# Kernel tuning notes

Hardware: AMD Instinct MI355X
Metric: run time of the kernel (lower is better)

The kernel has to match this reference:

```python
import jax, jax.numpy as jnp
import numpy as np

D = 256
H = 16
HD = D // H
N_BIAS = 6
B, E = 8, 1024


def _layernorm(x, g, b, eps=1e-5):
    mu = jnp.mean(x, axis=-1, keepdims=True)
    var = jnp.mean(jnp.square(x - mu), axis=-1, keepdims=True)
    return (x - mu) * jax.lax.rsqrt(var + eps) * g + b


def setup_inputs() -> dict:
    key = jax.random.key(0)
    ks = jax.random.split(key, 16)
    s = 0.02
    inp = {
        "x": jax.random.normal(ks[0], (B, E, D), dtype=jnp.float32),
        "struct_bias": jax.random.randint(ks[1], (B, E, E), 0, N_BIAS),
        "key_padding_mask": jnp.zeros((B, E), dtype=bool),
        # projections stored as [in, out] so y = x @ W + b
        "Wq": jax.random.normal(ks[2], (D, D), jnp.float32) * s,
        "bq": jnp.zeros((D,), jnp.float32),
        "Wk": jax.random.normal(ks[3], (D, D), jnp.float32) * s,
        "bk": jnp.zeros((D,), jnp.float32),
        "Wv": jax.random.normal(ks[4], (D, D), jnp.float32) * s,
        "bv": jnp.zeros((D,), jnp.float32),
        "Wo": jax.random.normal(ks[5], (D, D), jnp.float32) * s,
        "bo": jnp.zeros((D,), jnp.float32),
        "bias_emb": jax.random.normal(ks[6], (N_BIAS, H), jnp.float32) * s,
        "ln1_g": jnp.ones((D,), jnp.float32),
        "ln1_b": jnp.zeros((D,), jnp.float32),
        "W_ff1": jax.random.normal(ks[7], (D, 4 * D), jnp.float32) * s,
        "b_ff1": jnp.zeros((4 * D,), jnp.float32),
        "W_ff2": jax.random.normal(ks[8], (4 * D, D), jnp.float32) * s,
        "b_ff2": jnp.zeros((D,), jnp.float32),
        "ln2_g": jnp.ones((D,), jnp.float32),
        "ln2_b": jnp.zeros((D,), jnp.float32),
    }
    return inp


def reference(x, struct_bias, key_padding_mask, Wq, bq, Wk, bk, Wv, bv, Wo, bo,
              bias_emb, ln1_g, ln1_b, W_ff1, b_ff1, W_ff2, b_ff2, ln2_g, ln2_b):
    b, e, d = x.shape
    # project and split heads: [B, H, E, HD]
    q = (x @ Wq + bq).reshape(b, e, H, HD).transpose(0, 2, 1, 3)
    k = (x @ Wk + bk).reshape(b, e, H, HD).transpose(0, 2, 1, 3)
    v = (x @ Wv + bv).reshape(b, e, H, HD).transpose(0, 2, 1, 3)
    scores = jnp.einsum('bhqd,bhkd->bhqk', q, k) / np.sqrt(HD).astype(np.float32)
    # learned structural bias: [B,E,E,H] -> [B,H,E,E]
    bias = bias_emb[struct_bias].transpose(0, 3, 1, 2)
    scores = scores + bias
    scores = jnp.where(key_padding_mask[:, None, None, :], -jnp.inf, scores)
    attn = jax.nn.softmax(scores, axis=-1)
    out = jnp.einsum('bhqk,bhkd->bhqd', attn, v)
    out = out.transpose(0, 2, 1, 3).reshape(b, e, d)
    out = out @ Wo + bo
    x = _layernorm(x + out, ln1_g, ln1_b)
    ff = jax.nn.gelu(x @ W_ff1 + b_ff1, approximate=False) @ W_ff2 + b_ff2
    x = _layernorm(x + ff, ln2_g, ln2_b)
    return x
```

## Files before the change

### kernel.cpp

```cpp
#include <hip/hip_runtime.h>
#include <math.h>

#define B_  8
#define E_  1024
#define D_  256
#define H_  16
#define FF_ 1024
#define M_  (B_ * E_)

typedef __attribute__((ext_vector_type(8))) short short8;
typedef __attribute__((ext_vector_type(4))) float f32x4;
typedef unsigned short bf16u;

#define GLOAD_LDS16(g, l) __builtin_amdgcn_global_load_lds( \
    (const __attribute__((address_space(1))) void*)(g), \
    (__attribute__((address_space(3))) void*)(l), 16, 0, 0)

#define LGKM_BAR()  asm volatile("s_waitcnt lgkmcnt(0)\ns_barrier" ::: "memory")
#define VM_BAR(N)   asm volatile("s_waitcnt vmcnt(" #N ")\ns_barrier" ::: "memory")

__device__ __forceinline__ unsigned short f2bf(float f) {
  union { float f; unsigned u; } c; c.f = f;
  unsigned r = c.u + 0x7fffu + ((c.u >> 16) & 1u);
  return (unsigned short)(r >> 16);
}
__device__ __forceinline__ float gelu_exact(float x) {
  return 0.5f * x * (1.0f + erff(x * 0.70710678118654752f));
}

template<int K_, int EPI>
__global__ __launch_bounds__(256) void mm_p(
    const bf16u* __restrict__ A, const bf16u* __restrict__ Wt,
    const float* __restrict__ bias, void* __restrict__ Cout, int N)
{
  constexpr int BM = 128, BN = 64, KT = K_ / 64;
  constexpr int MT = 4, NT = 2;
  __shared__ bf16u As[2][BM * 64];
  __shared__ bf16u Bs[2][BN * 64];

  const int t = threadIdx.x;
  const int l15 = t & 15, quad = (t >> 4) & 3;
  const int w = t >> 6, wm = w >> 1, wn = w & 1;
  const int m0 = blockIdx.x * BM, n0 = blockIdx.y * BN;

  auto stage = [&](int kt, int pb) {
    const int k0 = kt * 64;
#pragma unroll
    for (int p = 0; p < 4; ++p) {
      int g = p * 256 + t;
      int m = g & 127, c = g >> 7;
      GLOAD_LDS16(A + (size_t)(m0 + m) * K_ + k0 + c * 8, &As[pb][g * 8]);
    }
#pragma unroll
    for (int p = 0; p < 2; ++p) {
      int g = p * 256 + t;
      int n = g & 63, c = g >> 6;
      GLOAD_LDS16(Wt + (size_t)(n0 + n) * K_ + k0 + c * 8, &Bs[pb][g * 8]);
    }
  };

  f32x4 acc[MT][NT];
  const f32x4 z4 = {0.f, 0.f, 0.f, 0.f};
#pragma unroll
  for (int i = 0; i < MT; ++i)
#pragma unroll
    for (int j = 0; j < NT; ++j) acc[i][j] = z4;

  stage(0, 0);
#pragma unroll
  for (int kt = 0; kt < KT; ++kt) {
    LGKM_BAR();
    if (kt + 1 < KT) { stage(kt + 1, (kt + 1) & 1); VM_BAR(6); }
    else             { VM_BAR(0); }
    const bf16u* Ab = As[kt & 1];
    const bf16u* Bb = Bs[kt & 1];
#pragma unroll
    for (int s = 0; s < 2; ++s) {
      const int cc = s * 4 + quad;
      short8 af[MT], bfr[NT];
#pragma unroll
      for (int mt = 0; mt < MT; ++mt)
        af[mt] = *(const short8*)(Ab + (cc * BM + wm * 64 + mt * 16 + l15) * 8);
#pragma unroll
      for (int nt = 0; nt < NT; ++nt)
        bfr[nt] = *(const short8*)(Bb + (cc * BN + wn * 32 + nt * 16 + l15) * 8);
#pragma unroll
      for (int mt = 0; mt < MT; ++mt)
#pragma unroll
        for (int nt = 0; nt < NT; ++nt)
          acc[mt][nt] = __builtin_amdgcn_mfma_f32_16x16x32_bf16(
              af[mt], bfr[nt], acc[mt][nt], 0, 0, 0);
    }
  }

#pragma unroll
  for (int mt = 0; mt < MT; ++mt) {
#pragma unroll
    for (int nt = 0; nt < NT; ++nt) {
      int col = n0 + wn * 32 + nt * 16 + l15;
      float bia = bias[col];
#pragma unroll
      for (int r = 0; r < 4; ++r) {
        int row = m0 + wm * 64 + mt * 16 + quad * 4 + r;
        size_t idx = (size_t)row * N + col;
        float v = acc[mt][nt][r] + bia;
        if (EPI == 2) ((bf16u*)Cout)[idx] = f2bf(gelu_exact(v));
        else          ((bf16u*)Cout)[idx] = f2bf(v);
      }
    }
  }
}

template<int K_, int LN1>
__global__ __launch_bounds__(256) void mm_ln_p(
    const bf16u* __restrict__ A, const bf16u* __restrict__ Wt,
    const float* __restrict__ bias, const float* __restrict__ R,
    const float* __restrict__ gam, const float* __restrict__ bet,
    float* __restrict__ Yf, bf16u* __restrict__ Yb)
{
  constexpr int KT = K_ / 64;
  __shared__ bf16u As[2][32 * 64];
  __shared__ bf16u Bs[2][256 * 64];
  __shared__ float red[2][32][4];

  const int t = threadIdx.x;
  const int l15 = t & 15, quad = (t >> 4) & 3;
  const int w = t >> 6;
  const int m0 = blockIdx.x * 32;

  auto stage = [&](int kt, int pb) {
    const int k0 = kt * 64;
    GLOAD_LDS16(A + (size_t)(m0 + (t & 31)) * K_ + k0 + (t >> 5) * 8,
                &As[pb][t * 8]);
#pragma unroll
    for (int p = 0; p < 8; ++p) {
      int g = p * 256 + t;
      GLOAD_LDS16(Wt + (size_t)(g & 255) * K_ + k0 + (g >> 8) * 8,
                  &Bs[pb][g * 8]);
    }
  };

  f32x4 acc[2][4];
  const f32x4 z4 = {0.f, 0.f, 0.f, 0.f};
#pragma unroll
  for (int i = 0; i < 2; ++i)
#pragma unroll
    for (int j = 0; j < 4; ++j) acc[i][j] = z4;

  stage(0, 0);
#pragma unroll
  for (int kt = 0; kt < KT; ++kt) {
    LGKM_BAR();
    if (kt + 1 < KT) { stage(kt + 1, (kt + 1) & 1); VM_BAR(9); }
    else             { VM_BAR(0); }
    const bf16u* Ab = As[kt & 1];
    const bf16u* Bb = Bs[kt & 1];
#pragma unroll
    for (int s = 0; s < 2; ++s) {
      const int cc = s * 4 + quad;
      short8 af[2], bfr[4];
#pragma unroll
      for (int mt = 0; mt < 2; ++mt)
        af[mt] = *(const short8*)(Ab + (cc * 32 + mt * 16 + l15) * 8);
#pragma unroll
      for (int nt = 0; nt < 4; ++nt)
        bfr[nt] = *(const short8*)(Bb + (cc * 256 + w * 64 + nt * 16 + l15) * 8);
#pragma unroll
      for (int mt = 0; mt < 2; ++mt)
#pragma unroll
        for (int nt = 0; nt < 4; ++nt)
          acc[mt][nt] = __builtin_amdgcn_mfma_f32_16x16x32_bf16(
              af[mt], bfr[nt], acc[mt][nt], 0, 0, 0);
    }
  }

  float ga[4], be4[4], bi[4];
#pragma unroll
  for (int nt = 0; nt < 4; ++nt) {
    int col = w * 64 + nt * 16 + l15;
    bi[nt] = bias[col]; ga[nt] = gam[col]; be4[nt] = bet[col];
  }
#pragma unroll
  for (int mt = 0; mt < 2; ++mt)
#pragma unroll
    for (int nt = 0; nt < 4; ++nt) {
      int col = w * 64 + nt * 16 + l15;
#pragma unroll
      for (int r = 0; r < 4; ++r) {
        int row = m0 + mt * 16 + quad * 4 + r;
        acc[mt][nt][r] += bi[nt] + R[(size_t)row * 256 + col];
      }
    }

  float s1[2][4], s2[2][4];
#pragma unroll
  for (int mt = 0; mt < 2; ++mt)
#pragma unroll
    for (int r = 0; r < 4; ++r) {
      float a = 0.f, b = 0.f;
#pragma unroll
      for (int nt = 0; nt < 4; ++nt) {
        float v = acc[mt][nt][r];
        a += v; b += v * v;
      }
      s1[mt][r] = a; s2[mt][r] = b;
    }
#pragma unroll
  for (int off = 1; off <= 8; off <<= 1)
#pragma unroll
    for (int mt = 0; mt < 2; ++mt)
#pragma unroll
      for (int r = 0; r < 4; ++r) {
        s1[mt][r] += __shfl_xor(s1[mt][r], off, 64);
        s2[mt][r] += __shfl_xor(s2[mt][r], off, 64);
      }
  if (l15 == 0) {
#pragma unroll
    for (int mt = 0; mt < 2; ++mt)
#pragma unroll
      for (int r = 0; r < 4; ++r) {
        int row32 = mt * 16 + quad * 4 + r;
        red[0][row32][w] = s1[mt][r];
        red[1][row32][w] = s2[mt][r];
      }
  }
  LGKM_BAR();

#pragma unroll
  for (int mt = 0; mt < 2; ++mt)
#pragma unroll
    for (int r = 0; r < 4; ++r) {
      int row32 = mt * 16 + quad * 4 + r;
      float4 sa = *(const float4*)&red[0][row32][0];
      float4 sb = *(const float4*)&red[1][row32][0];
      float sum = sa.x + sa.y + sa.z + sa.w;
      float sq  = sb.x + sb.y + sb.z + sb.w;
      float mu  = sum * (1.f / 256.f);
      float var = sq * (1.f / 256.f) - mu * mu;
      float rs  = 1.f / sqrtf(var + 1e-5f);
      int row = m0 + row32;
#pragma unroll
      for (int nt = 0; nt < 4; ++nt) {
        int col = w * 64 + nt * 16 + l15;
        float y = (acc[mt][nt][r] - mu) * rs * ga[nt] + be4[nt];
        size_t idx = (size_t)row * 256 + col;
        Yf[idx] = y;
        if (LN1) Yb[idx] = f2bf(y);
      }
    }
}

__global__ __launch_bounds__(256) void prep_k(
    const float* __restrict__ x, bf16u* __restrict__ xb,
    const float* __restrict__ Wq, const float* __restrict__ Wk,
    const float* __restrict__ Wv, const float* __restrict__ Wo,
    bf16u* __restrict__ Wqkvt, bf16u* __restrict__ Wot,
    const float* __restrict__ Wf1, bf16u* __restrict__ Wf1t,
    const float* __restrict__ Wf2, bf16u* __restrict__ Wf2t,
    const float* __restrict__ bq, const float* __restrict__ bk,
    const float* __restrict__ bv, float* __restrict__ bqkv)
{
  __shared__ float tile[32][33];
  const int bid = blockIdx.x;
  const int t = threadIdx.x;

  if (bid < 1024) {
    int i = bid * 256 + t;
    float4 a = ((const float4*)x)[i * 2];
    float4 b = ((const float4*)x)[i * 2 + 1];
    uint4 o;
    o.x = f2bf(a.x) | ((unsigned)f2bf(a.y) << 16);
    o.y = f2bf(a.z) | ((unsigned)f2bf(a.w) << 16);
    o.z = f2bf(b.x) | ((unsigned)f2bf(b.y) << 16);
    o.w = f2bf(b.z) | ((unsigned)f2bf(b.w) << 16);
    ((uint4*)xb)[i] = o;
  } else if (bid < 1792) {
    const float* src; bf16u* dst; int K, N, kb, nb;
    int rr = bid - 1024;
    if (rr < 256) {
      int z = rr >> 6, i = rr & 63;
      src = (z == 0) ? Wq : (z == 1) ? Wk : (z == 2) ? Wv : Wo;
      dst = (z == 0) ? Wqkvt : (z == 1) ? Wqkvt + 65536
          : (z == 2) ? Wqkvt + 131072 : Wot;
      K = 256; N = 256; kb = (i & 7) * 32; nb = (i >> 3) * 32;
    } else if (rr < 512) {
      int i = rr - 256;
      src = Wf1; dst = Wf1t; K = 256; N = 1024;
      kb = (i & 7) * 32; nb = (i >> 3) * 32;
    } else {
      int i = rr - 512;
      src = Wf2; dst = Wf2t; K = 1024; N = 256;
      kb = (i & 31) * 32; nb = (i >> 5) * 32;
    }
    const int tx = t & 31, ty = t >> 5;
#pragma unroll
    for (int r = 0; r < 4; ++r)
      tile[ty + 8 * r][tx] = src[(size_t)(kb + ty + 8 * r) * N + nb + tx];
    __syncthreads();
#pragma unroll
    for (int r = 0; r < 4; ++r)
      dst[(size_t)(nb + ty + 8 * r) * K + kb + tx] = f2bf(tile[tx][ty + 8 * r]);
  } else {
    for (int i = t; i < 768; i += 256)
      bqkv[i] = (i < 256) ? bq[i] : (i < 512) ? bk[i - 256] : bv[i - 512];
  }
}

__global__ __launch_bounds__(256) void attn_k(
    const bf16u* __restrict__ qkv, const int* __restrict__ sb,
    const unsigned char* __restrict__ mask, const float* __restrict__ be,
    bf16u* __restrict__ O)
{
  __shared__ bf16u Kl[2][64][40];
  __shared__ bf16u Vt[2][16][72];
  __shared__ bf16u Pl[4][16][40];
  __shared__ float embl[2][6];

  const int t    = threadIdx.x;
  const int b    = blockIdx.z;
  const int hg   = blockIdx.y;
  const int w    = t >> 6;
  const int lane = t & 63;
  const int l15  = lane & 15;
  const int quad = lane >> 4;
  const int q0w  = blockIdx.x * 64 + w * 16;

  if (t < 12) embl[t / 6][t % 6] = be[(t % 6) * 16 + hg * 2 + t / 6];

  {
    float4 z = {0.f, 0.f, 0.f, 0.f};
    float4* kp = (float4*)&Kl[0][0][0];
    for (int i = t; i < 640; i += 256) kp[i] = z;
  }

  short8 qf[2];
#pragma unroll
  for (int hp = 0; hp < 2; ++hp) {
    uint4 v = {0u, 0u, 0u, 0u};
    if (quad < 2)
      v = *(const uint4*)(qkv + ((size_t)(b * E_) + q0w + l15) * 768 +
                          (hg * 2 + hp) * 16 + quad * 8);
    else if (quad == 2)
      v.x = 0x3F80u;
    union { uint4 u; short8 s; } c; c.u = v;
    qf[hp] = c.s;
  }

  const int s_hp   = t >> 7;
  const int s_key  = (t >> 1) & 63;
  const int s_half = t & 1;
  const size_t kvbase = (size_t)b * E_ * 768;
  const int* sbp = sb + ((size_t)b * E_ + q0w) * E_;

  f32x4 accO[2];
  const f32x4 z4 = {0.f, 0.f, 0.f, 0.f};
  accO[0] = z4; accO[1] = z4;
  float lsum[2][4] = {};

  for (int k0 = 0; k0 < E_; k0 += 64) {
    int sbv[2][2][4];
#pragma unroll
    for (int s2 = 0; s2 < 2; ++s2)
#pragma unroll
      for (int f = 0; f < 2; ++f)
#pragma unroll
        for (int r = 0; r < 4; ++r)
          sbv[s2][f][r] = sbp[(size_t)(quad * 4 + r) * E_ + k0 + s2 * 32 + f * 16 + l15];

    __syncthreads();
    {
      const bf16u* kq = qkv + kvbase + (size_t)(k0 + s_key) * 768 + 256 +
                        (hg * 2 + s_hp) * 16 + s_half * 8;
      uint4 kw = *(const uint4*)kq;
      uint4 vw = *(const uint4*)(kq + 256);
      *(uint4*)&Kl[s_hp][s_key][s_half * 8] = kw;
      const int col = (s_key >> 5) * 32 + ((s_key & 15) << 1) + ((s_key >> 4) & 1);
      union { uint4 u; bf16u e[8]; } vc; vc.u = vw;
#pragma unroll
      for (int j = 0; j < 8; ++j)
        Vt[s_hp][s_half * 8 + j][col] = vc.e[j];
      if (s_half == 0) {
        unsigned char mv = mask[b * E_ + k0 + s_key];
        Kl[s_hp][s_key][16] = mv ? (bf16u)0xCF6E : (bf16u)0;
      }
    }
    __syncthreads();

#pragma unroll
    for (int hp = 0; hp < 2; ++hp) {
#pragma unroll
      for (int s2 = 0; s2 < 2; ++s2) {
        short8 kf0 = *(const short8*)&Kl[hp][s2 * 32 + l15][quad * 8];
        short8 kf1 = *(const short8*)&Kl[hp][s2 * 32 + 16 + l15][quad * 8];
        f32x4 sc0 = __builtin_amdgcn_mfma_f32_16x16x32_bf16(qf[hp], kf0, z4, 0, 0, 0);
        f32x4 sc1 = __builtin_amdgcn_mfma_f32_16x16x32_bf16(qf[hp], kf1, z4, 0, 0, 0);
#pragma unroll
        for (int r = 0; r < 4; ++r) {
          float w0 = embl[hp][sbv[s2][0][r]];
          float w1 = embl[hp][sbv[s2][1][r]];
          float p0 = __expf(fmaf(sc0[r], 0.25f, w0));
          float p1 = __expf(fmaf(sc1[r], 0.25f, w1));
          unsigned u0 = __float_as_uint(p0) & 0xffff0000u;
          unsigned u1 = __float_as_uint(p1) & 0xffff0000u;
          lsum[hp][r] += __uint_as_float(u0) + __uint_as_float(u1);
          *(unsigned*)&Pl[w][quad * 4 + r][l15 * 2] = (__float_as_uint(p0) >> 16) | u1;
        }
        short8 pf = *(const short8*)&Pl[w][l15][quad * 8];
        short8 vf = *(const short8*)&Vt[hp][l15][s2 * 32 + quad * 8];
        accO[hp] = __builtin_amdgcn_mfma_f32_16x16x32_bf16(pf, vf, accO[hp], 0, 0, 0);
      }
    }
  }

#pragma unroll
  for (int off = 1; off <= 8; off <<= 1)
#pragma unroll
    for (int hp = 0; hp < 2; ++hp)
#pragma unroll
      for (int r = 0; r < 4; ++r)
        lsum[hp][r] += __shfl_xor(lsum[hp][r], off, 64);

#pragma unroll
  for (int hp = 0; hp < 2; ++hp) {
#pragma unroll
    for (int r = 0; r < 4; ++r) {
      float o = accO[hp][r] / lsum[hp][r];
      O[((size_t)(b * E_) + q0w + quad * 4 + r) * 256 + (hg * 2 + hp) * 16 + l15] = f2bf(o);
    }
  }
}

extern "C" void kernel_launch(void* const* d_in, const int* in_sizes, int n_in,
                              void* d_out, int out_size, void* d_ws, size_t ws_size,
                              hipStream_t stream) {
  const float* x   = (const float*)d_in[0];
  const int*   sb  = (const int*)d_in[1];
  const unsigned char* mask = (const unsigned char*)d_in[2];
  const float* Wq  = (const float*)d_in[3];
  const float* bq  = (const float*)d_in[4];
  const float* Wk  = (const float*)d_in[5];
  const float* bk  = (const float*)d_in[6];
  const float* Wv  = (const float*)d_in[7];
  const float* bv  = (const float*)d_in[8];
  const float* Wo  = (const float*)d_in[9];
  const float* bo  = (const float*)d_in[10];
  const float* be  = (const float*)d_in[11];
  const float* g1  = (const float*)d_in[12];
  const float* b1  = (const float*)d_in[13];
  const float* Wf1 = (const float*)d_in[14];
  const float* bf1 = (const float*)d_in[15];
  const float* Wf2 = (const float*)d_in[16];
  const float* bf2 = (const float*)d_in[17];
  const float* g2  = (const float*)d_in[18];
  const float* b2  = (const float*)d_in[19];
  float* out = (float*)d_out;

  char* ws = (char*)d_ws;
  bf16u* Wqkvt = (bf16u*)(ws + 0);
  bf16u* Wot   = (bf16u*)(ws + 393216);
  bf16u* Wf1t  = (bf16u*)(ws + 524288);
  bf16u* Wf2t  = (bf16u*)(ws + 1048576);
  float* bqkv  = (float*)(ws + 1572864);
  bf16u* xb    = (bf16u*)(ws + 2097152);
  bf16u* qkv   = (bf16u*)(ws + 6291456);
  bf16u* att   = (bf16u*)(ws + 18874368);
  float* x1    = (float*)(ws + 23068672);
  bf16u* x1b   = (bf16u*)(ws + 31457280);
  bf16u* ffh   = (bf16u*)(ws + 2097152);

  dim3 blk(256);

  prep_k<<<1793, blk, 0, stream>>>(x, xb, Wq, Wk, Wv, Wo, Wqkvt, Wot,
                                   Wf1, Wf1t, Wf2, Wf2t, bq, bk, bv, bqkv);

  mm_p<256, 0><<<dim3(64, 12), blk, 0, stream>>>(xb, Wqkvt, bqkv, qkv, 768);

  attn_k<<<dim3(16, 8, 8), blk, 0, stream>>>(qkv, sb, mask, be, att);

  mm_ln_p<256, 1><<<256, blk, 0, stream>>>(att, Wot, bo, x, g1, b1, x1, x1b);

  mm_p<256, 2><<<dim3(64, 16), blk, 0, stream>>>(x1b, Wf1t, bf1, ffh, 1024);

  mm_ln_p<1024, 0><<<256, blk, 0, stream>>>(ffh, Wf2t, bf2, x1, g2, b2, out, nullptr);
}
```

Baseline: 244.9 us.

## Fuse FFN up-projection, GELU, down-projection and LayerNorm into one kernel

Replaces the separate FF1 GEMM (writing the bf16 hidden activations to global memory) and the FF2+LayerNorm kernel with a single kernel per 32-row tile. The 32x1024 GELU hidden tile is kept in LDS and consumed directly by the second GEMM. This removes the global write and read of the 16 MB hidden buffer and one launch. In exchange only 256 blocks run, each doing both GEMMs serially with heavy LDS use, which lowers parallelism and occupancy.

```diff
diff --git a/kernel.cpp b/kernel.cpp
--- a/kernel.cpp
+++ b/kernel.cpp
@@ -246,6 +246,192 @@
         size_t idx = (size_t)row * 256 + col;
         Yf[idx] = y;
         if (LN1) Yb[idx] = f2bf(y);
+      }
+    }
+}
+
+__global__ __launch_bounds__(256) void ffn_k(
+    const bf16u* __restrict__ x1b, const float* __restrict__ x1,
+    const bf16u* __restrict__ Wf1t, const float* __restrict__ bf1,
+    const bf16u* __restrict__ Wf2t, const float* __restrict__ bf2,
+    const float* __restrict__ g2, const float* __restrict__ b2,
+    float* __restrict__ out)
+{
+  __shared__ bf16u Bst[2][2048 * 8];
+  __shared__ bf16u ffh[32][1032];
+  __shared__ float red[2][32][4];
+  __shared__ float bfl[1024];
+  __shared__ float cst[3 * 256];
+
+  const int t = threadIdx.x;
+  const int l15 = t & 15, quad = (t >> 4) & 3;
+  const int w = t >> 6;
+  const int wm = w >> 1, wn = w & 1;
+  const int m0 = blockIdx.x * 32;
+
+  for (int i = t; i < 1024; i += 256) bfl[i] = bf1[i];
+  if (t < 256) { cst[t] = bf2[t]; cst[256 + t] = g2[t]; cst[512 + t] = b2[t]; }
+
+  short8 afx[8];
+  {
+    const bf16u* ap = x1b + (size_t)(m0 + wm * 16 + l15) * 256 + quad * 8;
+#pragma unroll
+    for (int s = 0; s < 8; ++s)
+      afx[s] = *(const short8*)(ap + s * 32);
+  }
+
+  auto stage1 = [&](int j, int pb) {
+#pragma unroll
+    for (int p = 0; p < 8; ++p) {
+      int g = p * 256 + t;
+      GLOAD_LDS16(Wf1t + (size_t)(j * 64 + (g & 63)) * 256 + (g >> 6) * 8,
+                  &Bst[pb][g * 8]);
+    }
+  };
+  auto stage2 = [&](int kt, int pb) {
+#pragma unroll
+    for (int p = 0; p < 8; ++p) {
+      int g = p * 256 + t;
+      GLOAD_LDS16(Wf2t + (size_t)(g & 255) * 1024 + kt * 64 + (g >> 8) * 8,
+                  &Bst[pb][g * 8]);
+    }
+  };
+
+  const f32x4 z4 = {0.f, 0.f, 0.f, 0.f};
+
+  stage1(0, 0);
+#pragma unroll
+  for (int j = 0; j < 16; ++j) {
+    LGKM_BAR();
+    if (j + 1 < 16) { stage1(j + 1, (j + 1) & 1); VM_BAR(8); }
+    else            { VM_BAR(0); }
+    const bf16u* Bb = Bst[j & 1];
+    f32x4 acc1[2] = {z4, z4};
+#pragma unroll
+    for (int s = 0; s < 8; ++s) {
+      const int cc = s * 4 + quad;
+      short8 bfr[2];
+#pragma unroll
+      for (int nt = 0; nt < 2; ++nt)
+        bfr[nt] = *(const short8*)(Bb + (cc * 64 + wn * 32 + nt * 16 + l15) * 8);
+#pragma unroll
+      for (int nt = 0; nt < 2; ++nt)
+        acc1[nt] = __builtin_amdgcn_mfma_f32_16x16x32_bf16(
+            afx[s], bfr[nt], acc1[nt], 0, 0, 0);
+    }
+#pragma unroll
+    for (int nt = 0; nt < 2; ++nt) {
+      int lcol = wn * 32 + nt * 16 + l15;
+      float bia = bfl[j * 64 + lcol];
+#pragma unroll
+      for (int r = 0; r < 4; ++r)
+        ffh[wm * 16 + quad * 4 + r][j * 64 + lcol] =
+            f2bf(gelu_exact(acc1[nt][r] + bia));
+    }
+  }
+
+  f32x4 acc[2][4];
+#pragma unroll
+  for (int i = 0; i < 2; ++i)
+#pragma unroll
+    for (int j = 0; j < 4; ++j) acc[i][j] = z4;
+
+  stage2(0, 0);
+#pragma unroll
+  for (int kt = 0; kt < 16; ++kt) {
+    LGKM_BAR();
+    if (kt + 1 < 16) { stage2(kt + 1, (kt + 1) & 1); VM_BAR(8); }
+    else             { VM_BAR(0); }
+    const bf16u* Bb = Bst[kt & 1];
+#pragma unroll
+    for (int s = 0; s < 2; ++s) {
+      const int cc = s * 4 + quad;
+      short8 af[2], bfr[4];
+#pragma unroll
+      for (int mt = 0; mt < 2; ++mt)
+        af[mt] = *(const short8*)&ffh[mt * 16 + l15][kt * 64 + s * 32 + quad * 8];
+#pragma unroll
+      for (int nt = 0; nt < 4; ++nt)
+        bfr[nt] = *(const short8*)(Bb + (cc * 256 + w * 64 + nt * 16 + l15) * 8);
+#pragma unroll
+      for (int mt = 0; mt < 2; ++mt)
+#pragma unroll
+        for (int nt = 0; nt < 4; ++nt)
+          acc[mt][nt] = __builtin_amdgcn_mfma_f32_16x16x32_bf16(
+              af[mt], bfr[nt], acc[mt][nt], 0, 0, 0);
+    }
+  }
+
+  float ga[4], be4[4], bi[4];
+#pragma unroll
+  for (int nt = 0; nt < 4; ++nt) {
+    int col = w * 64 + nt * 16 + l15;
+    bi[nt] = cst[col]; ga[nt] = cst[256 + col]; be4[nt] = cst[512 + col];
+  }
+#pragma unroll
+  for (int mt = 0; mt < 2; ++mt)
+#pragma unroll
+    for (int nt = 0; nt < 4; ++nt) {
+      int col = w * 64 + nt * 16 + l15;
+#pragma unroll
+      for (int r = 0; r < 4; ++r) {
+        int row = m0 + mt * 16 + quad * 4 + r;
+        acc[mt][nt][r] += bi[nt] + x1[(size_t)row * 256 + col];
+      }
+    }
+
+  float s1[2][4], s2[2][4];
+#pragma unroll
+  for (int mt = 0; mt < 2; ++mt)
+#pragma unroll
+    for (int r = 0; r < 4; ++r) {
+      float a = 0.f, b = 0.f;
+#pragma unroll
+      for (int nt = 0; nt < 4; ++nt) {
+        float v = acc[mt][nt][r];
+        a += v; b += v * v;
+      }
+      s1[mt][r] = a; s2[mt][r] = b;
+    }
+#pragma unroll
+  for (int off = 1; off <= 8; off <<= 1)
+#pragma unroll
+    for (int mt = 0; mt < 2; ++mt)
+#pragma unroll
+      for (int r = 0; r < 4; ++r) {
+        s1[mt][r] += __shfl_xor(s1[mt][r], off, 64);
+        s2[mt][r] += __shfl_xor(s2[mt][r], off, 64);
+      }
+  if (l15 == 0) {
+#pragma unroll
+    for (int mt = 0; mt < 2; ++mt)
+#pragma unroll
+      for (int r = 0; r < 4; ++r) {
+        int row32 = mt * 16 + quad * 4 + r;
+        red[0][row32][w] = s1[mt][r];
+        red[1][row32][w] = s2[mt][r];
+      }
+  }
+  LGKM_BAR();
+
+#pragma unroll
+  for (int mt = 0; mt < 2; ++mt)
+#pragma unroll
+    for (int r = 0; r < 4; ++r) {
+      int row32 = mt * 16 + quad * 4 + r;
+      float4 sa = *(const float4*)&red[0][row32][0];
+      float4 sb = *(const float4*)&red[1][row32][0];
+      float sum = sa.x + sa.y + sa.z + sa.w;
+      float sq  = sb.x + sb.y + sb.z + sb.w;
+      float mu  = sum * (1.f / 256.f);
+      float var = sq * (1.f / 256.f) - mu * mu;
+      float rs  = 1.f / sqrtf(var + 1e-5f);
+      int row = m0 + row32;
+#pragma unroll
+      for (int nt = 0; nt < 4; ++nt) {
+        int col = w * 64 + nt * 16 + l15;
+        float y = (acc[mt][nt][r] - mu) * rs * ga[nt] + be4[nt];
+        out[(size_t)row * 256 + col] = y;
       }
     }
 }
@@ -466,7 +652,6 @@
   bf16u* att   = (bf16u*)(ws + 18874368);
   float* x1    = (float*)(ws + 23068672);
   bf16u* x1b   = (bf16u*)(ws + 31457280);
-  bf16u* ffh   = (bf16u*)(ws + 2097152);
 
   dim3 blk(256);
 
@@ -479,7 +664,5 @@
 
   mm_ln_p<256, 1><<<256, blk, 0, stream>>>(att, Wot, bo, x, g1, b1, x1, x1b);
 
-  mm_p<256, 2><<<dim3(64, 16), blk, 0, stream>>>(x1b, Wf1t, bf1, ffh, 1024);
-
-  mm_ln_p<1024, 0><<<256, blk, 0, stream>>>(ffh, Wf2t, bf2, x1, g2, b2, out, nullptr);
-}
+  ffn_k<<<256, blk, 0, stream>>>(x1b, x1, Wf1t, bf1, Wf2t, bf2, g2, b2, out);
+}
```

Result: slower. 257.0 us (+4.9%).
